# Performance work log

Hardware: AMD Instinct MI355X
Metric: run time of the kernel (lower is better)

Reference implementation:

```python
import math
import jax, jax.numpy as jnp
import numpy as np

B, N, D_FULL, M, D_V = 8, 4096, 256, 256, 256


def _phi(x, omega):
    # x: [..., N, d_full], omega: [M, d_full] -> [..., N, M]
    proj = x @ omega.T
    log_phi = proj - 0.5 * jnp.sum(x * x, axis=-1, keepdims=True)
    log_phi = log_phi - jnp.max(log_phi, axis=-1, keepdims=True)
    return jnp.exp(log_phi) / math.sqrt(omega.shape[0])


def _causal(phi_q, phi_k, V):
    # phi_q/phi_k: [B, N, M], V: [B, N, d_v]
    b, n, m = phi_q.shape
    d_v = V.shape[-1]

    def step(carry, inp):
        S, z = carry
        pq, pk, v = inp  # [B,M], [B,M], [B,d_v]
        S = S + pk[:, :, None] * v[:, None, :]          # [B, M, d_v]
        z = z + pk                                       # [B, M]
        num = jnp.einsum('bi,bij->bj', pq, S)            # [B, d_v]
        den = jnp.maximum(jnp.sum(pq * z, axis=-1), 1e-6)
        return (S, z), num / den[:, None]

    S0 = jnp.zeros((b, m, d_v), phi_q.dtype)
    z0 = jnp.zeros((b, m), phi_q.dtype)
    xs = (jnp.swapaxes(phi_q, 0, 1), jnp.swapaxes(phi_k, 0, 1), jnp.swapaxes(V, 0, 1))
    _, ys = jax.lax.scan(step, (S0, z0), xs)  # ys: [N, B, d_v]
    return jnp.swapaxes(ys, 0, 1)


def setup_inputs() -> dict:
    key = jax.random.key(0)
    kq, kk, kv, ko = jax.random.split(key, 4)
    Q = jax.random.normal(kq, (B, N, D_FULL), dtype=jnp.float32)
    K_in = jax.random.normal(kk, (B, N, D_FULL), dtype=jnp.float32)
    V = jax.random.normal(kv, (B, N, D_V), dtype=jnp.float32)
    omega = jax.random.normal(ko, (M, D_FULL), dtype=jnp.float32)
    return {"Q": Q, "K_in": K_in, "V": V, "omega": omega, "causal": 1}


def reference(Q, K_in, V, omega, causal):
    phi_q = _phi(Q, omega)
    phi_k = _phi(K_in, omega)
    if causal:
        return _causal(phi_q, phi_k, V)
    S = jnp.einsum('bni,bnj->bij', phi_k, V)          # [B, M, d_v]
    z = jnp.sum(phi_k, axis=-2)                        # [B, M]
    num = jnp.einsum('bni,bij->bnj', phi_q, S)
    den = jnp.maximum(jnp.einsum('bni,bi->bn', phi_q, z), 1e-6)
    return num / den[..., None]
```

## Files before the change

kernel.cpp:

```cpp
#include <hip/hip_runtime.h>

#define BN 8
#define NN 4096
#define DD 256
#define MM 256
#define DV 256
#define CHUNK 256
#define NC (NN / CHUNK)

using f32x4 = __attribute__((ext_vector_type(4))) float;
using s16x8 = __attribute__((ext_vector_type(8))) short;

#define MFMA16(a, b, c) __builtin_amdgcn_mfma_f32_16x16x32_bf16(a, b, c, 0, 0, 0)

__device__ __forceinline__ unsigned short f2bf(float x) {
    union { float f; unsigned int u; } v; v.f = x;
    unsigned int r = v.u + 0x7FFF + ((v.u >> 16) & 1);
    return (unsigned short)(r >> 16);
}
__device__ __forceinline__ float bf2f(unsigned short u) {
    union { unsigned int u; float f; } v; v.u = ((unsigned int)u) << 16;
    return v.f;
}

__global__ __launch_bounds__(256) void omconv(
    const float* __restrict__ Om, unsigned short* __restrict__ OmH,
    unsigned short* __restrict__ OmL)
{
    const int i = blockIdx.x * 256 + threadIdx.x;
    const float4 v = *(const float4*)(Om + (size_t)i * 4);
    const float xs[4] = {v.x, v.y, v.z, v.w};
    unsigned short h[4], l[4];
#pragma unroll
    for (int j = 0; j < 4; ++j) {
        h[j] = f2bf(xs[j]);
        l[j] = f2bf(xs[j] - bf2f(h[j]));
    }
    *(uint2*)(OmH + (size_t)i * 4) = *(uint2*)h;
    *(uint2*)(OmL + (size_t)i * 4) = *(uint2*)l;
}

template<bool KPATH>
__global__ __launch_bounds__(256) void phi_mfma(
    const float* __restrict__ X, const unsigned short* __restrict__ OmH,
    const unsigned short* __restrict__ OmL, unsigned short* __restrict__ Phi,
    unsigned short* __restrict__ PhiT, float* __restrict__ Zp)
{
    const int tid = threadIdx.x;
    const int w = tid >> 6;
    const int lane = tid & 63;
    const int col = lane & 15, quad = lane >> 4;
    const long r0 = (long)blockIdx.x * 64;

    __shared__ __align__(16) char lds[33792];
    __shared__ float rowmax_s[64];
    short (*Xh)[40] = (short(*)[40])lds;
    short (*Xl)[40] = (short(*)[40])(lds + 5120);
    float (*red)[67] = (float(*)[67])lds;
    unsigned short (*P)[264] = (unsigned short(*)[264])lds;
    unsigned int* P32 = (unsigned int*)lds;

    f32x4 acc[4][4] = {};
    const int srow = tid >> 2;
    const int sk = (tid & 3) * 8;

    for (int kt = 0; kt < DD; kt += 32) {
        const float4 v0 = *(const float4*)(X + (r0 + srow) * DD + kt + sk);
        const float4 v1 = *(const float4*)(X + (r0 + srow) * DD + kt + sk + 4);
        const float xs[8] = {v0.x, v0.y, v0.z, v0.w, v1.x, v1.y, v1.z, v1.w};
        unsigned short h[8], l[8];
#pragma unroll
        for (int j = 0; j < 8; ++j) {
            h[j] = f2bf(xs[j]);
            l[j] = f2bf(xs[j] - bf2f(h[j]));
        }
        __syncthreads();
        *(uint4*)&Xh[srow][sk] = *(uint4*)h;
        *(uint4*)&Xl[srow][sk] = *(uint4*)l;
        __syncthreads();

        s16x8 ah[4], al[4], bh[4], bl[4];
#pragma unroll
        for (int t = 0; t < 4; ++t) {
            ah[t] = *(const s16x8*)&Xh[t * 16 + col][quad * 8];
            al[t] = *(const s16x8*)&Xl[t * 16 + col][quad * 8];
        }
#pragma unroll
        for (int ct = 0; ct < 4; ++ct) {
            const size_t off = (size_t)(w * 64 + ct * 16 + col) * DD + kt + quad * 8;
            bh[ct] = *(const s16x8*)(OmH + off);
            bl[ct] = *(const s16x8*)(OmL + off);
        }
#pragma unroll
        for (int t = 0; t < 4; ++t)
#pragma unroll
            for (int ct = 0; ct < 4; ++ct) {
                acc[t][ct] = MFMA16(ah[t], bh[ct], acc[t][ct]);
                acc[t][ct] = MFMA16(ah[t], bl[ct], acc[t][ct]);
                acc[t][ct] = MFMA16(al[t], bh[ct], acc[t][ct]);
            }
    }

    __syncthreads();
#pragma unroll
    for (int t = 0; t < 4; ++t)
#pragma unroll
        for (int r = 0; r < 4; ++r) {
            float m = acc[t][0][r];
#pragma unroll
            for (int ct = 1; ct < 4; ++ct) m = fmaxf(m, acc[t][ct][r]);
            red[t * 16 + quad * 4 + r][w * 16 + col] = m;
        }
    __syncthreads();
    if (tid < 64) {
        float m = red[tid][0];
#pragma unroll
        for (int j = 1; j < 64; ++j) m = fmaxf(m, red[tid][j]);
        rowmax_s[tid] = m;
    }
    __syncthreads();

#pragma unroll
    for (int t = 0; t < 4; ++t)
#pragma unroll
        for (int r = 0; r < 4; ++r) {
            const int n = t * 16 + quad * 4 + r;
            const float rm = rowmax_s[n];
#pragma unroll
            for (int ct = 0; ct < 4; ++ct) {
                const float val = __expf(acc[t][ct][r] - rm) * 0.0625f;
                const unsigned u = (unsigned)f2bf(val);
                const unsigned up = (unsigned)__shfl_xor((int)u, 1);
                if ((col & 1) == 0)
                    P32[n * 132 + w * 32 + ct * 8 + (col >> 1)] = u | (up << 16);
            }
        }
    __syncthreads();

    {
        const int t7 = tid & 7;
        const int nb = tid >> 3;
#pragma unroll
        for (int p2 = 0; p2 < 2; ++p2) {
            const int n = p2 * 32 + nb;
#pragma unroll
            for (int s = 0; s < 4; ++s)
                *(uint4*)(Phi + (r0 + n) * MM + t7 * 8 + s * 64) =
                    *(const uint4*)&P[n][t7 * 8 + s * 64];
        }
    }

    if (KPATH) {
        const int b = blockIdx.x >> 6;
        const int c = (blockIdx.x >> 2) & 15;
        const int n0 = (int)(r0 & (NN - 1));
        const int m0 = tid & 31;
        const int nsub = tid >> 5;
#pragma unroll
        for (int mi = 0; mi < 8; ++mi) {
            const int m = mi * 32 + m0;
            unsigned short u[8];
#pragma unroll
            for (int j = 0; j < 8; ++j) u[j] = P[nsub * 8 + j][m];
            *(uint4*)(PhiT + ((size_t)b * MM + m) * NN + n0 + nsub * 8) = *(uint4*)u;
        }
        float z = 0.f;
#pragma unroll
        for (int n = 0; n < 64; ++n) z += bf2f(P[n][tid]);
        atomicAdd(&Zp[((b * NC + c) << 8) + tid], z);
    }
}

__global__ __launch_bounds__(256) void transpose_v(
    const float* __restrict__ V, unsigned short* __restrict__ VT)
{
    const int tid = threadIdx.x;
    const int ct = blockIdx.x & 3;
    const long r0 = (long)(blockIdx.x >> 2) * 64;
    const int b = (int)(r0 >> 12);
    const int n0 = (int)(r0 & (NN - 1));
    __shared__ unsigned short T[64][72];
    const int rr = tid >> 4, cs = tid & 15;
#pragma unroll
    for (int p = 0; p < 4; ++p) {
        const int r = p * 16 + rr;
        const float4 v = *(const float4*)(V + (r0 + r) * DV + ct * 64 + cs * 4);
        T[cs * 4 + 0][r] = f2bf(v.x); T[cs * 4 + 1][r] = f2bf(v.y);
        T[cs * 4 + 2][r] = f2bf(v.z); T[cs * 4 + 3][r] = f2bf(v.w);
    }
    __syncthreads();
    const int cl = tid >> 3, ns = tid & 7;
#pragma unroll
    for (int p = 0; p < 2; ++p) {
        const int c = p * 32 + cl;
        *(uint4*)(VT + ((size_t)b * DV + ct * 64 + c) * NN + n0 + ns * 8) = *(uint4*)&T[c][ns * 8];
    }
}

__global__ __launch_bounds__(256) void state_mfma(
    const unsigned short* __restrict__ VT, const unsigned short* __restrict__ PkT,
    unsigned short* __restrict__ ST)
{
    const int tid = threadIdx.x;
    const int w = tid >> 6;
    const int lane = tid & 63;
    const int col = lane & 15, quad = lane >> 4;
    const int q = blockIdx.x & 3;
    const int c = (blockIdx.x >> 2) & (NC - 1);
    const int b = blockIdx.x >> 6;
    const int dv0 = (q & 1) * 128 + (w & 1) * 64;
    const int m0  = (q >> 1) * 128 + (w >> 1) * 64;
    const unsigned short* Ab = VT  + (size_t)b * DV * NN + (size_t)c * CHUNK;
    const unsigned short* Bb = PkT + (size_t)b * MM * NN + (size_t)c * CHUNK;

    f32x4 acc[4][4] = {};
    for (int kr = 0; kr < CHUNK; kr += 32) {
        s16x8 a[4], bb[4];
#pragma unroll
        for (int t = 0; t < 4; ++t)
            a[t] = *(const s16x8*)(Ab + (size_t)(dv0 + t * 16 + col) * NN + kr + quad * 8);
#pragma unroll
        for (int t = 0; t < 4; ++t)
            bb[t] = *(const s16x8*)(Bb + (size_t)(m0 + t * 16 + col) * NN + kr + quad * 8);
#pragma unroll
        for (int i = 0; i < 4; ++i)
#pragma unroll
            for (int j = 0; j < 4; ++j) acc[i][j] = MFMA16(a[i], bb[j], acc[i][j]);
    }
    unsigned short* Sb = ST + (((size_t)(b * NC + c)) << 16);
#pragma unroll
    for (int i = 0; i < 4; ++i)
#pragma unroll
        for (int j = 0; j < 4; ++j)
#pragma unroll
            for (int r = 0; r < 4; ++r)
                Sb[(dv0 + i * 16 + quad * 4 + r) * MM + m0 + j * 16 + col] = f2bf(acc[i][j][r]);
}

__global__ __launch_bounds__(256) void prefix2(
    unsigned short* __restrict__ ST, float* __restrict__ Z)
{
    const long idx = (long)blockIdx.x * 256 + threadIdx.x;
    const int b = (int)(idx >> 16);
    const int r = (int)(idx & 65535);
    float run = 0.f;
#pragma unroll
    for (int c = 0; c < NC; ++c) {
        const size_t off = (((size_t)(b * NC + c)) << 16) + r;
        const float v = bf2f(ST[off]);
        ST[off] = f2bf(run);
        run += v;
    }
    if (idx < BN * MM) {
        const int b2 = (int)(idx >> 8);
        const int m = (int)(idx & 255);
        float rz = 0.f;
#pragma unroll
        for (int c = 0; c < NC; ++c) {
            const size_t off = (size_t)(b2 * NC + c) * MM + m;
            const float v = Z[off];
            Z[off] = rz;
            rz += v;
        }
    }
}

__global__ __launch_bounds__(256) void out_mfma(
    const unsigned short* __restrict__ PhiQ, const unsigned short* __restrict__ PhiK,
    const unsigned short* __restrict__ VT, const unsigned short* __restrict__ ST,
    const float* __restrict__ Z, float* __restrict__ Out)
{
    const int tid = threadIdx.x;
    const int w = tid >> 6;
    const int lane = tid & 63;
    const int col = lane & 15, quad = lane >> 4;
    const int it = 3 - ((blockIdx.x >> 7) & 3);
    const int low = blockIdx.x & 127;
    const int c  = low & 15;
    const int b  = low >> 4;
    const size_t chunk_row = (size_t)b * NN + (size_t)c * CHUNK;
    const unsigned short* Qrow = PhiQ + (chunk_row + it * 64) * MM;

    __shared__ unsigned short A_s[64][72];
    __shared__ float red[64][68];
    __shared__ float z_s[256];
    __shared__ float den_s[64];

    f32x4 oacc[4][4] = {};
    float rsum[4][4] = {};

    for (int jt = 0; jt <= it; ++jt) {
        const unsigned short* Krow = PhiK + (chunk_row + jt * 64) * MM;
        f32x4 accA[4] = {};
        for (int m = 0; m < MM; m += 32) {
            const s16x8 bk = *(const s16x8*)(Krow + (w * 16 + col) * MM + m + quad * 8);
#pragma unroll
            for (int t = 0; t < 4; ++t) {
                const s16x8 aq = *(const s16x8*)(Qrow + (t * 16 + col) * MM + m + quad * 8);
                accA[t] = MFMA16(aq, bk, accA[t]);
            }
        }
        __syncthreads();
#pragma unroll
        for (int t = 0; t < 4; ++t)
#pragma unroll
            for (int r = 0; r < 4; ++r) {
                const int i_loc = t * 16 + quad * 4 + r;
                const int j_loc = w * 16 + col;
                float v = (jt * 64 + j_loc <= it * 64 + i_loc) ? accA[t][r] : 0.f;
                rsum[t][r] += v;
                A_s[i_loc][j_loc] = f2bf(v);
            }
        __syncthreads();
#pragma unroll
        for (int ks = 0; ks < 64; ks += 32) {
            s16x8 av[4];
#pragma unroll
            for (int t = 0; t < 4; ++t)
                av[t] = *(const s16x8*)(&A_s[t * 16 + col][ks + quad * 8]);
#pragma unroll
            for (int t2 = 0; t2 < 4; ++t2) {
                const s16x8 bv = *(const s16x8*)(VT + ((size_t)b * DV + w * 64 + t2 * 16 + col) * NN
                                                 + (size_t)c * CHUNK + jt * 64 + ks + quad * 8);
#pragma unroll
                for (int t = 0; t < 4; ++t) oacc[t][t2] = MFMA16(av[t], bv, oacc[t][t2]);
            }
        }
    }
#pragma unroll
    for (int t = 0; t < 4; ++t)
#pragma unroll
        for (int r = 0; r < 4; ++r)
            red[t * 16 + quad * 4 + r][w * 16 + col] = rsum[t][r];
    z_s[tid] = Z[((size_t)(b * NC + c) << 8) + tid];
    __syncthreads();
    const unsigned short* Sb = ST + (((size_t)(b * NC + c)) << 16);
    for (int m = 0; m < MM; m += 32) {
        s16x8 aq[4];
#pragma unroll
        for (int t = 0; t < 4; ++t)
            aq[t] = *(const s16x8*)(Qrow + (t * 16 + col) * MM + m + quad * 8);
#pragma unroll
        for (int t2 = 0; t2 < 4; ++t2) {
            const s16x8 bs = *(const s16x8*)(Sb + (w * 64 + t2 * 16 + col) * MM + m + quad * 8);
#pragma unroll
            for (int t = 0; t < 4; ++t) oacc[t][t2] = MFMA16(aq[t], bs, oacc[t][t2]);
        }
    }
    {
        const int i = tid & 63;
        const int seg = tid >> 6;
        float d = 0.f;
#pragma unroll
        for (int k = 0; k < 64; k += 8) {
            unsigned short u[8];
            *(uint4*)u = *(const uint4*)(Qrow + i * MM + seg * 64 + k);
#pragma unroll
            for (int x = 0; x < 8; ++x) d = fmaf(bf2f(u[x]), z_s[seg * 64 + k + x], d);
        }
        red[i][64 + seg] = d;
    }
    __syncthreads();
    if (tid < 64) {
        float s = 0.f;
#pragma unroll
        for (int j = 0; j < 68; ++j) s += red[tid][j];
        den_s[tid] = fmaxf(s, 1e-6f);
    }
    __syncthreads();
#pragma unroll
    for (int t = 0; t < 4; ++t)
#pragma unroll
        for (int r = 0; r < 4; ++r) {
            const int i_loc = t * 16 + quad * 4 + r;
            const float invd = 1.0f / den_s[i_loc];
#pragma unroll
            for (int t2 = 0; t2 < 4; ++t2)
                Out[(chunk_row + it * 64 + i_loc) * DV + w * 64 + t2 * 16 + col] = oacc[t][t2][r] * invd;
        }
}

extern "C" void kernel_launch(void* const* d_in, const int* in_sizes, int n_in,
                              void* d_out, int out_size, void* d_ws, size_t ws_size,
                              hipStream_t stream)
{
    const float* Q  = (const float*)d_in[0];
    const float* K  = (const float*)d_in[1];
    const float* V  = (const float*)d_in[2];
    const float* Om = (const float*)d_in[3];
    float* out = (float*)d_out;

    const size_t NM = (size_t)BN * NN * MM;
    unsigned short* PhiQ  = (unsigned short*)d_ws;
    unsigned short* PhiK  = PhiQ + NM;
    unsigned short* PhiKT = PhiK + NM;
    unsigned short* VT    = PhiKT + NM;
    unsigned short* ST    = VT + NM;
    unsigned short* OmH   = ST + (size_t)BN * NC * DV * MM;
    unsigned short* OmL   = OmH + (size_t)MM * DD;
    float* Z = (float*)(OmL + (size_t)MM * DD);

    hipMemsetAsync(Z, 0, (size_t)BN * NC * MM * sizeof(float), stream);
    omconv<<<dim3(64), dim3(256), 0, stream>>>(Om, OmH, OmL);
    phi_mfma<false><<<dim3((BN * NN) / 64), dim3(256), 0, stream>>>(Q, OmH, OmL, PhiQ, nullptr, nullptr);
    phi_mfma<true><<<dim3((BN * NN) / 64), dim3(256), 0, stream>>>(K, OmH, OmL, PhiK, PhiKT, Z);
    transpose_v<<<dim3((BN * NN) / 64 * 4), dim3(256), 0, stream>>>(V, VT);
    state_mfma<<<dim3(BN * NC * 4), dim3(256), 0, stream>>>(VT, PhiKT, ST);
    prefix2<<<dim3((BN * DV * MM) / 256), dim3(256), 0, stream>>>(ST, Z);
    out_mfma<<<dim3(BN * NC * 4), dim3(256), 0, stream>>>(PhiQ, PhiK, VT, ST, Z, out);
}
```

Measured before the change: 266.8 us.

## Stage inputs in LDS and software-pipeline global operand loads across MFMA kernels

phi_mfma now loads and splits the whole 64x256 X tile into LDS once, replacing the per-k-step load/sync loop, and double-buffers the omega fragment loads in registers. state_mfma prefetches the next k-slice into registers, reorders block indexing so the quadrant index is outermost, and adds an occupancy hint to launch_bounds. out_mfma caches the Q tile in LDS, prefetches the next K tile and the V fragments, and double-buffers the S loads, which removes repeated global Q reads. This trades higher LDS and register use, and so lower occupancy, for fewer barriers and more load/compute overlap.

```diff
diff --git a/kernel.cpp b/kernel.cpp
--- a/kernel.cpp
+++ b/kernel.cpp
@@ -52,53 +52,69 @@
     const int col = lane & 15, quad = lane >> 4;
     const long r0 = (long)blockIdx.x * 64;
 
-    __shared__ __align__(16) char lds[33792];
+    __shared__ __align__(16) char lds[67584];
     __shared__ float rowmax_s[64];
-    short (*Xh)[40] = (short(*)[40])lds;
-    short (*Xl)[40] = (short(*)[40])(lds + 5120);
-    float (*red)[67] = (float(*)[67])lds;
+    short (*Xh)[264] = (short(*)[264])lds;
+    short (*Xl)[264] = (short(*)[264])(lds + 33792);
     unsigned short (*P)[264] = (unsigned short(*)[264])lds;
     unsigned int* P32 = (unsigned int*)lds;
+    float (*red)[67] = (float(*)[67])(lds + 34048);
+
+    float4 xv[16];
+#pragma unroll
+    for (int i = 0; i < 16; ++i)
+        xv[i] = *(const float4*)(X + r0 * DD + (size_t)(i * 256 + tid) * 4);
+#pragma unroll
+    for (int i = 0; i < 16; ++i) {
+        const int f = i * 256 + tid;
+        const int row = f >> 6;
+        const int k4 = (f & 63) * 4;
+        const float xs[4] = {xv[i].x, xv[i].y, xv[i].z, xv[i].w};
+        unsigned short hh[4], ll[4];
+#pragma unroll
+        for (int j = 0; j < 4; ++j) {
+            hh[j] = f2bf(xs[j]);
+            ll[j] = f2bf(xs[j] - bf2f(hh[j]));
+        }
+        *(uint2*)&Xh[row][k4] = *(uint2*)hh;
+        *(uint2*)&Xl[row][k4] = *(uint2*)ll;
+    }
+    __syncthreads();
 
     f32x4 acc[4][4] = {};
-    const int srow = tid >> 2;
-    const int sk = (tid & 3) * 8;
-
-    for (int kt = 0; kt < DD; kt += 32) {
-        const float4 v0 = *(const float4*)(X + (r0 + srow) * DD + kt + sk);
-        const float4 v1 = *(const float4*)(X + (r0 + srow) * DD + kt + sk + 4);
-        const float xs[8] = {v0.x, v0.y, v0.z, v0.w, v1.x, v1.y, v1.z, v1.w};
-        unsigned short h[8], l[8];
-#pragma unroll
-        for (int j = 0; j < 8; ++j) {
-            h[j] = f2bf(xs[j]);
-            l[j] = f2bf(xs[j] - bf2f(h[j]));
-        }
-        __syncthreads();
-        *(uint4*)&Xh[srow][sk] = *(uint4*)h;
-        *(uint4*)&Xl[srow][sk] = *(uint4*)l;
-        __syncthreads();
-
-        s16x8 ah[4], al[4], bh[4], bl[4];
+    s16x8 bh0[4], bl0[4], bh1[4], bl1[4];
+#pragma unroll
+    for (int ct = 0; ct < 4; ++ct) {
+        const size_t off = (size_t)(w * 64 + ct * 16 + col) * DD + quad * 8;
+        bh0[ct] = *(const s16x8*)(OmH + off);
+        bl0[ct] = *(const s16x8*)(OmL + off);
+    }
+#pragma unroll
+    for (int kt = 0; kt < 8; ++kt) {
+        if (kt < 7) {
+#pragma unroll
+            for (int ct = 0; ct < 4; ++ct) {
+                const size_t off = (size_t)(w * 64 + ct * 16 + col) * DD + (kt + 1) * 32 + quad * 8;
+                bh1[ct] = *(const s16x8*)(OmH + off);
+                bl1[ct] = *(const s16x8*)(OmL + off);
+            }
+        }
+        s16x8 ah[4], al[4];
 #pragma unroll
         for (int t = 0; t < 4; ++t) {
-            ah[t] = *(const s16x8*)&Xh[t * 16 + col][quad * 8];
-            al[t] = *(const s16x8*)&Xl[t * 16 + col][quad * 8];
-        }
-#pragma unroll
-        for (int ct = 0; ct < 4; ++ct) {
-            const size_t off = (size_t)(w * 64 + ct * 16 + col) * DD + kt + quad * 8;
-            bh[ct] = *(const s16x8*)(OmH + off);
-            bl[ct] = *(const s16x8*)(OmL + off);
+            ah[t] = *(const s16x8*)&Xh[t * 16 + col][kt * 32 + quad * 8];
+            al[t] = *(const s16x8*)&Xl[t * 16 + col][kt * 32 + quad * 8];
         }
 #pragma unroll
         for (int t = 0; t < 4; ++t)
 #pragma unroll
             for (int ct = 0; ct < 4; ++ct) {
-                acc[t][ct] = MFMA16(ah[t], bh[ct], acc[t][ct]);
-                acc[t][ct] = MFMA16(ah[t], bl[ct], acc[t][ct]);
-                acc[t][ct] = MFMA16(al[t], bh[ct], acc[t][ct]);
-            }
+                acc[t][ct] = MFMA16(ah[t], bh0[ct], acc[t][ct]);
+                acc[t][ct] = MFMA16(ah[t], bl0[ct], acc[t][ct]);
+                acc[t][ct] = MFMA16(al[t], bh0[ct], acc[t][ct]);
+            }
+#pragma unroll
+        for (int ct = 0; ct < 4; ++ct) { bh0[ct] = bh1[ct]; bl0[ct] = bl1[ct]; }
     }
 
     __syncthreads();
@@ -197,7 +213,7 @@
     }
 }
 
-__global__ __launch_bounds__(256) void state_mfma(
+__global__ __launch_bounds__(256, 3) void state_mfma(
     const unsigned short* __restrict__ VT, const unsigned short* __restrict__ PkT,
     unsigned short* __restrict__ ST)
 {
@@ -205,27 +221,37 @@
     const int w = tid >> 6;
     const int lane = tid & 63;
     const int col = lane & 15, quad = lane >> 4;
-    const int q = blockIdx.x & 3;
-    const int c = (blockIdx.x >> 2) & (NC - 1);
-    const int b = blockIdx.x >> 6;
+    const int q  = blockIdx.x >> 7;
+    const int bc = blockIdx.x & 127;
+    const int c  = bc & 15;
+    const int b  = bc >> 4;
     const int dv0 = (q & 1) * 128 + (w & 1) * 64;
     const int m0  = (q >> 1) * 128 + (w >> 1) * 64;
     const unsigned short* Ab = VT  + (size_t)b * DV * NN + (size_t)c * CHUNK;
     const unsigned short* Bb = PkT + (size_t)b * MM * NN + (size_t)c * CHUNK;
 
     f32x4 acc[4][4] = {};
-    for (int kr = 0; kr < CHUNK; kr += 32) {
-        s16x8 a[4], bb[4];
-#pragma unroll
-        for (int t = 0; t < 4; ++t)
-            a[t] = *(const s16x8*)(Ab + (size_t)(dv0 + t * 16 + col) * NN + kr + quad * 8);
-#pragma unroll
-        for (int t = 0; t < 4; ++t)
-            bb[t] = *(const s16x8*)(Bb + (size_t)(m0 + t * 16 + col) * NN + kr + quad * 8);
+    s16x8 a0[4], b0[4], a1[4], b1[4];
+#pragma unroll
+    for (int t = 0; t < 4; ++t) {
+        a0[t] = *(const s16x8*)(Ab + (size_t)(dv0 + t * 16 + col) * NN + quad * 8);
+        b0[t] = *(const s16x8*)(Bb + (size_t)(m0 + t * 16 + col) * NN + quad * 8);
+    }
+#pragma unroll
+    for (int kt = 0; kt < 8; ++kt) {
+        if (kt < 7) {
+#pragma unroll
+            for (int t = 0; t < 4; ++t) {
+                a1[t] = *(const s16x8*)(Ab + (size_t)(dv0 + t * 16 + col) * NN + (kt + 1) * 32 + quad * 8);
+                b1[t] = *(const s16x8*)(Bb + (size_t)(m0 + t * 16 + col) * NN + (kt + 1) * 32 + quad * 8);
+            }
+        }
 #pragma unroll
         for (int i = 0; i < 4; ++i)
 #pragma unroll
-            for (int j = 0; j < 4; ++j) acc[i][j] = MFMA16(a[i], bb[j], acc[i][j]);
+            for (int j = 0; j < 4; ++j) acc[i][j] = MFMA16(a0[i], b0[j], acc[i][j]);
+#pragma unroll
+        for (int t = 0; t < 4; ++t) { a0[t] = a1[t]; b0[t] = b1[t]; }
     }
     unsigned short* Sb = ST + (((size_t)(b * NC + c)) << 16);
 #pragma unroll
@@ -274,31 +300,60 @@
     const int w = tid >> 6;
     const int lane = tid & 63;
     const int col = lane & 15, quad = lane >> 4;
-    const int it = 3 - ((blockIdx.x >> 7) & 3);
+    const int it = 3 - (blockIdx.x >> 7);
     const int low = blockIdx.x & 127;
     const int c  = low & 15;
     const int b  = low >> 4;
     const size_t chunk_row = (size_t)b * NN + (size_t)c * CHUNK;
     const unsigned short* Qrow = PhiQ + (chunk_row + it * 64) * MM;
 
+    __shared__ unsigned short Qs[64][264];
     __shared__ unsigned short A_s[64][72];
     __shared__ float red[64][68];
     __shared__ float z_s[256];
     __shared__ float den_s[64];
 
+    const float zval = Z[((size_t)(b * NC + c) << 8) + tid];
+    s16x8 bk0[8], bk1[8];
+#pragma unroll
+    for (int ms = 0; ms < 8; ++ms)
+        bk0[ms] = *(const s16x8*)(PhiK + (chunk_row)*MM + (size_t)(w * 16 + col) * MM + ms * 32 + quad * 8);
+    uint4 qv[8];
+#pragma unroll
+    for (int i = 0; i < 8; ++i)
+        qv[i] = *((const uint4*)Qrow + i * 256 + tid);
+    z_s[tid] = zval;
+#pragma unroll
+    for (int i = 0; i < 8; ++i) {
+        const int f = i * 256 + tid;
+        *(uint4*)&Qs[f >> 5][(f & 31) * 8] = qv[i];
+    }
+    __syncthreads();
+
     f32x4 oacc[4][4] = {};
     float rsum[4][4] = {};
 
     for (int jt = 0; jt <= it; ++jt) {
-        const unsigned short* Krow = PhiK + (chunk_row + jt * 64) * MM;
+        s16x8 bv[8];
+        const unsigned short* Vbase = VT + ((size_t)b * DV + w * 64) * NN + (size_t)c * CHUNK + jt * 64;
+#pragma unroll
+        for (int ks2 = 0; ks2 < 2; ++ks2)
+#pragma unroll
+            for (int t2 = 0; t2 < 4; ++t2)
+                bv[ks2 * 4 + t2] = *(const s16x8*)(Vbase + (size_t)(t2 * 16 + col) * NN + ks2 * 32 + quad * 8);
         f32x4 accA[4] = {};
-        for (int m = 0; m < MM; m += 32) {
-            const s16x8 bk = *(const s16x8*)(Krow + (w * 16 + col) * MM + m + quad * 8);
+#pragma unroll
+        for (int ms = 0; ms < 8; ++ms)
 #pragma unroll
             for (int t = 0; t < 4; ++t) {
-                const s16x8 aq = *(const s16x8*)(Qrow + (t * 16 + col) * MM + m + quad * 8);
-                accA[t] = MFMA16(aq, bk, accA[t]);
-            }
+                const s16x8 aq = *(const s16x8*)&Qs[t * 16 + col][ms * 32 + quad * 8];
+                accA[t] = MFMA16(aq, bk0[ms], accA[t]);
+            }
+        if (jt < it) {
+            const unsigned short* Krn = PhiK + (chunk_row + (jt + 1) * 64) * MM;
+#pragma unroll
+            for (int ms = 0; ms < 8; ++ms)
+                bk1[ms] = *(const s16x8*)(Krn + (size_t)(w * 16 + col) * MM + ms * 32 + quad * 8);
         }
         __syncthreads();
 #pragma unroll
@@ -313,50 +368,60 @@
             }
         __syncthreads();
 #pragma unroll
-        for (int ks = 0; ks < 64; ks += 32) {
+        for (int ks2 = 0; ks2 < 2; ++ks2) {
             s16x8 av[4];
 #pragma unroll
             for (int t = 0; t < 4; ++t)
-                av[t] = *(const s16x8*)(&A_s[t * 16 + col][ks + quad * 8]);
-#pragma unroll
-            for (int t2 = 0; t2 < 4; ++t2) {
-                const s16x8 bv = *(const s16x8*)(VT + ((size_t)b * DV + w * 64 + t2 * 16 + col) * NN
-                                                 + (size_t)c * CHUNK + jt * 64 + ks + quad * 8);
-#pragma unroll
-                for (int t = 0; t < 4; ++t) oacc[t][t2] = MFMA16(av[t], bv, oacc[t][t2]);
-            }
-        }
+                av[t] = *(const s16x8*)&A_s[t * 16 + col][ks2 * 32 + quad * 8];
+#pragma unroll
+            for (int t2 = 0; t2 < 4; ++t2)
+#pragma unroll
+                for (int t = 0; t < 4; ++t)
+                    oacc[t][t2] = MFMA16(av[t], bv[ks2 * 4 + t2], oacc[t][t2]);
+        }
+#pragma unroll
+        for (int ms = 0; ms < 8; ++ms) bk0[ms] = bk1[ms];
     }
 #pragma unroll
     for (int t = 0; t < 4; ++t)
 #pragma unroll
         for (int r = 0; r < 4; ++r)
             red[t * 16 + quad * 4 + r][w * 16 + col] = rsum[t][r];
-    z_s[tid] = Z[((size_t)(b * NC + c) << 8) + tid];
-    __syncthreads();
-    const unsigned short* Sb = ST + (((size_t)(b * NC + c)) << 16);
-    for (int m = 0; m < MM; m += 32) {
+
+    const unsigned short* Sb = ST + (((size_t)(b * NC + c)) << 16) + (size_t)(w * 64) * MM;
+    s16x8 bs0[4], bs1[4];
+#pragma unroll
+    for (int t2 = 0; t2 < 4; ++t2)
+        bs0[t2] = *(const s16x8*)(Sb + (size_t)(t2 * 16 + col) * MM + quad * 8);
+#pragma unroll
+    for (int ms = 0; ms < 8; ++ms) {
+        if (ms < 7) {
+#pragma unroll
+            for (int t2 = 0; t2 < 4; ++t2)
+                bs1[t2] = *(const s16x8*)(Sb + (size_t)(t2 * 16 + col) * MM + (ms + 1) * 32 + quad * 8);
+        }
         s16x8 aq[4];
 #pragma unroll
         for (int t = 0; t < 4; ++t)
-            aq[t] = *(const s16x8*)(Qrow + (t * 16 + col) * MM + m + quad * 8);
-#pragma unroll
-        for (int t2 = 0; t2 < 4; ++t2) {
-            const s16x8 bs = *(const s16x8*)(Sb + (w * 64 + t2 * 16 + col) * MM + m + quad * 8);
-#pragma unroll
-            for (int t = 0; t < 4; ++t) oacc[t][t2] = MFMA16(aq[t], bs, oacc[t][t2]);
-        }
+            aq[t] = *(const s16x8*)&Qs[t * 16 + col][ms * 32 + quad * 8];
+#pragma unroll
+        for (int t2 = 0; t2 < 4; ++t2)
+#pragma unroll
+            for (int t = 0; t < 4; ++t)
+                oacc[t][t2] = MFMA16(aq[t], bs0[t2], oacc[t][t2]);
+#pragma unroll
+        for (int t2 = 0; t2 < 4; ++t2) bs0[t2] = bs1[t2];
     }
     {
         const int i = tid & 63;
         const int seg = tid >> 6;
         float d = 0.f;
 #pragma unroll
-        for (int k = 0; k < 64; k += 8) {
-            unsigned short u[8];
-            *(uint4*)u = *(const uint4*)(Qrow + i * MM + seg * 64 + k);
-#pragma unroll
-            for (int x = 0; x < 8; ++x) d = fmaf(bf2f(u[x]), z_s[seg * 64 + k + x], d);
+        for (int g = 0; g < 8; ++g) {
+            const s16x8 qv8 = *(const s16x8*)&Qs[i][seg * 64 + g * 8];
+#pragma unroll
+            for (int x = 0; x < 8; ++x)
+                d = fmaf(bf2f((unsigned short)qv8[x]), z_s[seg * 64 + g * 8 + x], d);
         }
         red[i][64 + seg] = d;
     }
```

Measured after the change: 253.6 us. -4.9%, faster.
